# Kernel tuning notes

Measured on AMD Instinct MI355X. Metric: run time of the kernel, lower is better.

The kernel has to match this reference:

```python
import jax, jax.numpy as jnp
import numpy as np

SQRT3 = 1.7320508075688772
SQRT3_2 = 0.8660254037844386
SQRT3_3 = 0.5773502691896257

N_POINTS = 8388608
CAM_RINGS = 24      # hex camera rings -> 3*R^2+3*R+1 = 1801 pixels
KERNEL_RINGS = 1    # splat stencil rings -> 7 neighbor offsets
SIGMA = 0.5


def _build_sensor():
    """Precompute the static (eqx.field(static=True)) sensor geometry, faithfully
    reproducing _detect_hex_grid / _build_lookup_table / _hex_neighbor_offsets."""
    R = CAM_RINGS
    qs = [(q, r) for q in range(-R, R + 1) for r in range(-R, R + 1)
          if max(abs(q), abs(r), abs(q + r)) <= R]
    q = np.array([a for a, _ in qs], np.float64)
    r = np.array([b for _, b in qs], np.float64)
    centers = np.stack([SQRT3 * (q + r / 2.0), 1.5 * r], axis=1)  # pointy-top, size=1
    n = len(centers)
    # _detect_hex_grid
    diff = centers[:, None, :] - centers[None, :, :]
    dist_sq = (diff ** 2).sum(-1)
    np.fill_diagonal(dist_sq, np.inf)
    min_dist = np.sqrt(dist_sq.min())
    i, j = np.unravel_index(np.argmin(dist_sq), dist_sq.shape)
    vec = centers[i] - centers[j]
    rot = float(np.mod(np.arctan2(vec[1], vec[0]), np.pi / 3.0))
    offset = centers[np.argmin((centers ** 2).sum(1))]
    hex_size = float(min_dist / SQRT3)
    # _build_lookup_table
    xs = centers[:, 0] - offset[0]
    ys = centers[:, 1] - offset[1]
    c, s = np.cos(-rot), np.sin(-rot)
    xr = c * xs - s * ys
    yr = s * xs + c * ys
    qf = (SQRT3_3 * xr - yr / 3.0) / hex_size
    rf = 2.0 * yr / 3.0 / hex_size
    qi = np.round(qf).astype(np.int32)
    ri = np.round(rf).astype(np.int32)
    q_min, r_min = int(qi.min()), int(ri.min())
    table = np.full((int(qi.max()) - q_min + 1, int(ri.max()) - r_min + 1), -1, np.int32)
    table[qi - q_min, ri - r_min] = np.arange(n, dtype=np.int32)
    # _hex_neighbor_offsets
    K = KERNEL_RINGS
    offs = [(a, b) for a in range(-K, K + 1) for b in range(-K, K + 1)
            if max(abs(a), abs(b), abs(a + b)) <= K]
    nq = np.array([o[0] for o in offs], np.int32)
    nr = np.array([o[1] for o in offs], np.int32)
    ox = (hex_size * SQRT3 * (nq + nr / 2.0)).astype(np.float32)
    oy = (hex_size * 1.5 * nr).astype(np.float32)
    return dict(
        lookup_table=jnp.asarray(table),
        neighbor_q=jnp.asarray(nq), neighbor_r=jnp.asarray(nr),
        neighbor_ox=jnp.asarray(ox), neighbor_oy=jnp.asarray(oy),
        hex_size=hex_size, hex_inradius=hex_size * SQRT3_2,
        grid_rotation=rot, grid_offset=(float(offset[0]), float(offset[1])),
        q_min=q_min, r_min=r_min, n_pixels=n,
    )

SENSOR = _build_sensor()


def _axial_round(q, r):
    s = -q - r
    qi, ri, si = jnp.round(q), jnp.round(r), jnp.round(s)
    dq, dr, ds = jnp.abs(qi - q), jnp.abs(ri - r), jnp.abs(si - s)
    qi = jnp.where((dq > dr) & (dq > ds), -ri - si, qi)
    ri = jnp.where((dr > dq) & (dr > ds), -qi - si, ri)
    return qi, ri


def setup_inputs() -> dict:
    key = jax.random.key(0)
    k1, k2, k3 = jax.random.split(key, 3)
    # camera footprint half-extent ~ SQRT3*CAM_RINGS; sample mostly inside
    L = 0.6 * SQRT3 * CAM_RINGS
    x = jax.random.uniform(k1, (N_POINTS,), jnp.float32, -L, L)
    y = jax.random.uniform(k2, (N_POINTS,), jnp.float32, -L, L)
    values = jax.random.normal(k3, (N_POINTS,), jnp.float32)
    return {"x": x, "y": y, "values": values}


def reference(x, y, values):
    S = SENSOR
    hs = S["hex_size"]
    inr = S["hex_inradius"]
    # rotate into grid frame by -grid_rotation
    c = jnp.cos(-S["grid_rotation"]).astype(x.dtype) if False else np.float32(np.cos(-S["grid_rotation"]))
    s = np.float32(np.sin(-S["grid_rotation"]))
    xs = x - np.float32(S["grid_offset"][0])
    ys = y - np.float32(S["grid_offset"][1])
    x_g = c * xs - s * ys
    y_g = s * xs + c * ys
    # cartesian -> fractional axial -> nearest hex center
    q = (SQRT3_3 * x_g - y_g / 3.0) / hs
    r = 2.0 * y_g / 3.0 / hs
    q_base, r_base = _axial_round(q, r)
    base_x = hs * SQRT3 * (q_base + r_base / 2.0)
    base_y = hs * 1.5 * r_base
    dx = x_g - base_x
    dy = y_g - base_y
    # neighbor stencil: [P, 7]
    qi = q_base[:, None].astype(jnp.int32) + S["neighbor_q"]
    ri = r_base[:, None].astype(jnp.int32) + S["neighbor_r"]
    dist_x = dx[:, None] - S["neighbor_ox"]
    dist_y = dy[:, None] - S["neighbor_oy"]
    hex_dist = jnp.maximum(jnp.abs(dist_y),
                           SQRT3_2 * jnp.abs(dist_x) + 0.5 * jnp.abs(dist_y)) / inr
    weights = jnp.exp(-0.5 * (hex_dist / SIGMA) ** 2)
    weights = weights / weights.sum(axis=1, keepdims=True)
    # lookup-table gather with bounds masking
    tbl = S["lookup_table"]
    q_idx = qi - S["q_min"]
    r_idx = ri - S["r_min"]
    in_bounds = (q_idx >= 0) & (q_idx < tbl.shape[0]) & (r_idx >= 0) & (r_idx < tbl.shape[1])
    q_safe = jnp.clip(q_idx, 0, tbl.shape[0] - 1)
    r_safe = jnp.clip(r_idx, 0, tbl.shape[1] - 1)
    pixel_idx = tbl[q_safe, r_safe]
    valid = in_bounds & (pixel_idx >= 0)
    pixel_idx = jnp.where(valid, pixel_idx, 0)
    splatted = values[:, None] * weights * valid
    return jax.ops.segment_sum(splatted.reshape(-1), pixel_idx.reshape(-1),
                               num_segments=S["n_pixels"])
```

## Files before the change

### kernel.cpp

```cpp
#include <hip/hip_runtime.h>
#include <hip/hip_bf16.h>

#define NPIX 1801
#define NT   256
#define NB   2048
#define MAXSLICES 32

#define FXSCALE 1048576.0f
#define FXINV   (1.0f / 1048576.0f)
#define KHD 1.9614249f
#define KHX 1.6986436f
#define C1  1.4710687f
#define C2  2.9421374f

__device__ __forceinline__ int col_base(int q) {
    int a = q + 24;
    return (q <= 0) ? (a * 26 + ((a * (a - 1)) >> 1))
                    : (900 + 49 * q - ((q * (q - 1)) >> 1));
}

__device__ __forceinline__ bool in_hex(int q, int r) {
    return (unsigned)(q + 24) <= 48u && (unsigned)(r + 24) <= 48u &&
           (unsigned)(q + r + 24) <= 48u;
}

__device__ __forceinline__ void splat_point(float px, float py, float pv,
                                            unsigned int* hist)
{
    float q = fmaf(-0.33333334f, py, 0.57735027f * px);
    float r = 0.66666669f * py;

    float sn = -q - r;
    float qi = rintf(q), ri = rintf(r), si = rintf(sn);
    float dq = fabsf(qi - q), dr = fabsf(ri - r), ds = fabsf(si - sn);
    if (dq > dr && dq > ds)      qi = -ri - si;
    else if (dr > dq && dr > ds) ri = -qi - si;

    int qb = (int)qi;
    int rb = (int)ri;

    float dx = fmaf(-1.7320508f, fmaf(0.5f, ri, qi), px);
    float dy = fmaf(-1.5f, ri, py);

    float Y  = KHD * dy;
    float X  = KHX * dx;
    float Ym = Y - C2, Yp = Y + C2;
    float Xm = X - C1, Xp = X + C1;
    float XM = X - C2, XP = X + C2;
    float h0 = 0.5f * fabsf(Y);
    float hm = 0.5f * fabsf(Ym);
    float hp = 0.5f * fabsf(Yp);
    float u0 = fmaxf(fabsf(Y),  fabsf(XP) + h0);
    float u1 = fmaxf(fabsf(Ym), fabsf(Xp) + hm);
    float u2 = fmaxf(fabsf(Yp), fabsf(Xp) + hp);
    float u3 = fmaxf(fabsf(Y),  fabsf(X)  + h0);
    float u4 = fmaxf(fabsf(Ym), fabsf(Xm) + hm);
    float u5 = fmaxf(fabsf(Yp), fabsf(Xm) + hp);
    float u6 = fmaxf(fabsf(Y),  fabsf(XM) + h0);
    float w0 = __builtin_amdgcn_exp2f(-(u0 * u0));
    float w1 = __builtin_amdgcn_exp2f(-(u1 * u1));
    float w2 = __builtin_amdgcn_exp2f(-(u2 * u2));
    float w3 = __builtin_amdgcn_exp2f(-(u3 * u3));
    float w4 = __builtin_amdgcn_exp2f(-(u4 * u4));
    float w5 = __builtin_amdgcn_exp2f(-(u5 * u5));
    float w6 = __builtin_amdgcn_exp2f(-(u6 * u6));
    float wsum = ((w0 + w1) + (w2 + w3)) + ((w4 + w5) + w6);
    float vinv = (pv * FXSCALE) * __builtin_amdgcn_rcpf(wsum);

    bool interior = (fabsf(qi) <= 23.0f) & (fabsf(ri) <= 23.0f) &
                    (fabsf(qi + ri) <= 23.0f);
    if (__builtin_expect(interior, 1)) {
        int m  = qb < 0 ? -qb : qb;
        int t  = (m * (99 - m)) >> 1;
        int b1 = 900 + rb + (qb < 0 ? -t : t);
        int t2 = qb + qb;
        int a0 = t2 - 1; a0 = a0 < 0 ? -a0 : a0;
        int a2 = t2 + 1; a2 = a2 < 0 ? -a2 : a2;
        int A0 = b1 - ((99 - a0) >> 1);
        int A2 = b1 + ((99 - a2) >> 1);
        atomicAdd(&hist[A0],     (unsigned int)(int)(w0 * vinv));
        atomicAdd(&hist[A0 + 1], (unsigned int)(int)(w1 * vinv));
        atomicAdd(&hist[b1 - 1], (unsigned int)(int)(w2 * vinv));
        atomicAdd(&hist[b1],     (unsigned int)(int)(w3 * vinv));
        atomicAdd(&hist[b1 + 1], (unsigned int)(int)(w4 * vinv));
        atomicAdd(&hist[A2 - 1], (unsigned int)(int)(w5 * vinv));
        atomicAdd(&hist[A2],     (unsigned int)(int)(w6 * vinv));
    } else {
        const int nq_[7] = {-1, -1, 0, 0, 0, 1, 1};
        const int nr_[7] = {0, 1, -1, 0, 1, -1, 0};
        float warr[7] = {w0, w1, w2, w3, w4, w5, w6};
        #pragma unroll
        for (int nn = 0; nn < 7; ++nn) {
            int qn = qb + nq_[nn];
            int rn = rb + nr_[nn];
            if (in_hex(qn, rn)) {
                atomicAdd(&hist[col_base(qn) + rn],
                          (unsigned int)(int)(warr[nn] * vinv));
            }
        }
    }
}

__global__ __launch_bounds__(NT) void hexsplat_kernel(
    const float* __restrict__ xs, const float* __restrict__ ys,
    const float* __restrict__ vs, unsigned int* __restrict__ acc,
    int n4, int slice_mask)
{
    const int t0 = blockIdx.x * NT + threadIdx.x;
    const int stride = NB * NT;
    const float4* x4 = (const float4*)xs;
    const float4* y4 = (const float4*)ys;
    const float4* v4 = (const float4*)vs;

    __shared__ unsigned int hist[NPIX];
    #pragma unroll 4
    for (int i = threadIdx.x; i < NPIX; i += NT) hist[i] = 0u;

    float4 xc, yc, vc;
    bool havec = t0 < n4;
    if (havec) { xc = x4[t0]; yc = y4[t0]; vc = v4[t0]; }
    __syncthreads();

    for (int i = t0; i < n4; i += stride) {
        float4 xn, yn, vn;
        int inext = i + stride;
        bool haven = inext < n4;
        if (haven) { xn = x4[inext]; yn = y4[inext]; vn = v4[inext]; }
        #pragma unroll
        for (int k = 0; k < 4; ++k)
            splat_point((&xc.x)[k], (&yc.x)[k], (&vc.x)[k], hist);
        xc = xn; yc = yn; vc = vn;
    }

    __syncthreads();
    unsigned int* aslice = acc + (size_t)(blockIdx.x & slice_mask) * NPIX;
    for (int i = threadIdx.x; i < NPIX; i += NT) {
        atomicAdd(&aslice[i], hist[i]);
    }
}

__global__ void finalize_kernel(const unsigned int* __restrict__ acc,
                                float* __restrict__ out, int nslices)
{
    int i = blockIdx.x * blockDim.x + threadIdx.x;
    if (i < NPIX) {
        unsigned int s = 0;
        for (int k = 0; k < nslices; ++k) s += acc[(size_t)k * NPIX + i];
        out[i] = (float)(int)s * FXINV;
    }
}

extern "C" void kernel_launch(void* const* d_in, const int* in_sizes, int n_in,
                              void* d_out, int out_size, void* d_ws, size_t ws_size,
                              hipStream_t stream) {
    const float* x = (const float*)d_in[0];
    const float* y = (const float*)d_in[1];
    const float* v = (const float*)d_in[2];
    float* out = (float*)d_out;
    unsigned int* acc = (unsigned int*)d_ws;
    int n = in_sizes[0];
    int n4 = n / 4;

    int nslices = 1;
    while (nslices < MAXSLICES &&
           (size_t)(nslices * 2) * NPIX * sizeof(unsigned int) <= ws_size)
        nslices *= 2;

    hipMemsetAsync(acc, 0, (size_t)nslices * NPIX * sizeof(unsigned int), stream);
    hexsplat_kernel<<<NB, NT, 0, stream>>>(x, y, v, acc, n4, nslices - 1);
    finalize_kernel<<<(NPIX + 255) / 256, 256, 0, stream>>>(acc, out, nslices);
}
```

Measured before the change: 132.2 us.

## Flush block histograms directly to output with float atomics, drop finalize kernel

Removes the sliced integer accumulator and the separate finalize kernel. Each block now converts its fixed-point shared histogram to float and atomically adds it into the zeroed output with unsafeAtomicAdd. The launch shape changes to 1024 blocks of 512 threads, so fewer blocks flush to global memory, and the hex-distance math is rewritten to use fmaf. This saves one kernel launch and the slice reduction, but every block's flush now contends on a single output array, and summing in float makes the result order-dependent.

Measured after the change: 138.1 us. +4.5%, slower.

```diff
diff --git a/kernel.cpp b/kernel.cpp
--- a/kernel.cpp
+++ b/kernel.cpp
@@ -2,9 +2,8 @@
 #include <hip/hip_bf16.h>
 
 #define NPIX 1801
-#define NT   256
-#define NB   2048
-#define MAXSLICES 32
+#define NT   512
+#define NB   1024
 
 #define FXSCALE 1048576.0f
 #define FXINV   (1.0f / 1048576.0f)
@@ -47,16 +46,16 @@
     float Ym = Y - C2, Yp = Y + C2;
     float Xm = X - C1, Xp = X + C1;
     float XM = X - C2, XP = X + C2;
-    float h0 = 0.5f * fabsf(Y);
-    float hm = 0.5f * fabsf(Ym);
-    float hp = 0.5f * fabsf(Yp);
-    float u0 = fmaxf(fabsf(Y),  fabsf(XP) + h0);
-    float u1 = fmaxf(fabsf(Ym), fabsf(Xp) + hm);
-    float u2 = fmaxf(fabsf(Yp), fabsf(Xp) + hp);
-    float u3 = fmaxf(fabsf(Y),  fabsf(X)  + h0);
-    float u4 = fmaxf(fabsf(Ym), fabsf(Xm) + hm);
-    float u5 = fmaxf(fabsf(Yp), fabsf(Xm) + hp);
-    float u6 = fmaxf(fabsf(Y),  fabsf(XM) + h0);
+    float aY = fabsf(Y), aYm = fabsf(Ym), aYp = fabsf(Yp);
+    float aX = fabsf(X), aXm = fabsf(Xm), aXp = fabsf(Xp);
+    float aXM = fabsf(XM), aXP = fabsf(XP);
+    float u0 = fmaxf(aY,  fmaf(0.5f, aY,  aXP));
+    float u1 = fmaxf(aYm, fmaf(0.5f, aYm, aXp));
+    float u2 = fmaxf(aYp, fmaf(0.5f, aYp, aXp));
+    float u3 = fmaxf(aY,  fmaf(0.5f, aY,  aX));
+    float u4 = fmaxf(aYm, fmaf(0.5f, aYm, aXm));
+    float u5 = fmaxf(aYp, fmaf(0.5f, aYp, aXm));
+    float u6 = fmaxf(aY,  fmaf(0.5f, aY,  aXM));
     float w0 = __builtin_amdgcn_exp2f(-(u0 * u0));
     float w1 = __builtin_amdgcn_exp2f(-(u1 * u1));
     float w2 = __builtin_amdgcn_exp2f(-(u2 * u2));
@@ -103,8 +102,7 @@
 
 __global__ __launch_bounds__(NT) void hexsplat_kernel(
     const float* __restrict__ xs, const float* __restrict__ ys,
-    const float* __restrict__ vs, unsigned int* __restrict__ acc,
-    int n4, int slice_mask)
+    const float* __restrict__ vs, float* __restrict__ out, int n4)
 {
     const int t0 = blockIdx.x * NT + threadIdx.x;
     const int stride = NB * NT;
@@ -133,20 +131,9 @@
     }
 
     __syncthreads();
-    unsigned int* aslice = acc + (size_t)(blockIdx.x & slice_mask) * NPIX;
     for (int i = threadIdx.x; i < NPIX; i += NT) {
-        atomicAdd(&aslice[i], hist[i]);
-    }
-}
-
-__global__ void finalize_kernel(const unsigned int* __restrict__ acc,
-                                float* __restrict__ out, int nslices)
-{
-    int i = blockIdx.x * blockDim.x + threadIdx.x;
-    if (i < NPIX) {
-        unsigned int s = 0;
-        for (int k = 0; k < nslices; ++k) s += acc[(size_t)k * NPIX + i];
-        out[i] = (float)(int)s * FXINV;
+        float f = (float)(int)hist[i] * FXINV;
+        unsafeAtomicAdd(&out[i], f);
     }
 }
 
@@ -157,16 +144,9 @@
     const float* y = (const float*)d_in[1];
     const float* v = (const float*)d_in[2];
     float* out = (float*)d_out;
-    unsigned int* acc = (unsigned int*)d_ws;
     int n = in_sizes[0];
     int n4 = n / 4;
 
-    int nslices = 1;
-    while (nslices < MAXSLICES &&
-           (size_t)(nslices * 2) * NPIX * sizeof(unsigned int) <= ws_size)
-        nslices *= 2;
-
-    hipMemsetAsync(acc, 0, (size_t)nslices * NPIX * sizeof(unsigned int), stream);
-    hexsplat_kernel<<<NB, NT, 0, stream>>>(x, y, v, acc, n4, nslices - 1);
-    finalize_kernel<<<(NPIX + 255) / 256, 256, 0, stream>>>(acc, out, nslices);
+    hipMemsetAsync(out, 0, (size_t)out_size * sizeof(float), stream);
+    hexsplat_kernel<<<NB, NT, 0, stream>>>(x, y, v, out, n4);
 }
```
